# Optimization experiments

Measured on AMD Instinct MI355X. Metric: run time of the kernel, lower is better.

The kernel has to match this reference:

```python
import jax, jax.numpy as jnp
import numpy as np
import math

N, J = 8192, 22  # N = batch*frames (per-frame calls are independent), J = num_joint


def _layernorm(x, g, b, eps=1e-5):
    m = jnp.mean(x, axis=-1, keepdims=True)
    v = jnp.var(x, axis=-1, keepdims=True)
    return (x - m) * jax.lax.rsqrt(v + eps) * g + b


def _attention(x, Wqkv, bqkv, Wo, bo, heads):
    # x: [B, n, d]; matches torch Attention (scale = d**-0.5)
    B, n, d = x.shape
    hd = d // heads
    qkv = (x @ Wqkv + bqkv).reshape(B, n, 3, heads, hd).transpose(2, 0, 3, 1, 4)
    q, k, v = qkv[0], qkv[1], qkv[2]  # [B, h, n, hd]
    dots = jnp.einsum('bhid,bhjd->bhij', q, k) * (d ** -0.5)
    attn = jax.nn.softmax(dots, axis=-1)
    out = jnp.einsum('bhij,bhjd->bhid', attn, v)
    out = out.transpose(0, 2, 1, 3).reshape(B, n, -1)
    return out @ Wo + bo


def _encoder(x, tok_W, tok_b, qkv_W, qkv_b, o_W, o_b, ln_g, ln_b, m1_W, m1_b, m2_W, m2_b, heads):
    tok = x @ tok_W + tok_b                                   # [B, J, 64]
    h = _attention(tok, qkv_W, qkv_b, o_W, o_b, heads)        # [B, J, out_dim]
    hn = _layernorm(h, ln_g, ln_b)
    mlp = jax.nn.relu(hn @ m1_W + m1_b) @ m2_W + m2_b
    return h + mlp                                            # Residual(LN+MLP)


def _sinusoidal_pe(max_len, dim):
    pos = np.arange(max_len)[:, None].astype(np.float32)
    div = np.exp(np.arange(0, dim, 2, dtype=np.float32) * (-math.log(10000.0) / dim))
    pe = np.zeros((max_len, dim), dtype=np.float32)
    pe[:, 0::2] = np.sin(pos * div)
    pe[:, 1::2] = np.cos(pos * div)
    return jnp.asarray(pe)


def setup_inputs() -> dict:
    key = jax.random.key(0)
    ks = iter(jax.random.split(key, 64))
    rn = lambda shape, s=0.1: jax.random.normal(next(ks), shape, dtype=jnp.float32) * s
    inp = {
        'q_t': jax.random.normal(next(ks), (N, J, 4), dtype=jnp.float32),
        'skelA': jax.random.normal(next(ks), (N, J, 3), dtype=jnp.float32),
        'skelB': jax.random.normal(next(ks), (N, J, 3), dtype=jnp.float32),
        'quat_mean': jax.random.normal(next(ks), (J, 4), dtype=jnp.float32) * 0.1,
        'quat_std': jax.random.uniform(next(ks), (J, 4), dtype=jnp.float32, minval=0.5, maxval=1.5),
        # QuatEncoder params
        'qe_tok_W': rn((4, 64)), 'qe_tok_b': jnp.zeros((64,), jnp.float32),
        'qe_qkv_W': rn((64, 192)), 'qe_qkv_b': jnp.zeros((192,), jnp.float32),
        'qe_o_W': rn((64, 256)), 'qe_o_b': jnp.zeros((256,), jnp.float32),
        'qe_ln_g': jnp.ones((256,), jnp.float32), 'qe_ln_b': jnp.zeros((256,), jnp.float32),
        'qe_m1_W': rn((256, 512)), 'qe_m1_b': jnp.zeros((512,), jnp.float32),
        'qe_m2_W': rn((512, 256)), 'qe_m2_b': jnp.zeros((256,), jnp.float32),
        # shared SeklEncoder params
        'se_tok_W': rn((3, 64)), 'se_tok_b': jnp.zeros((64,), jnp.float32),
        'se_qkv_W': rn((64, 192)), 'se_qkv_b': jnp.zeros((192,), jnp.float32),
        'se_o_W': rn((64, 128)), 'se_o_b': jnp.zeros((128,), jnp.float32),
        'se_ln_g': jnp.ones((128,), jnp.float32), 'se_ln_b': jnp.zeros((128,), jnp.float32),
        'se_m1_W': rn((128, 256)), 'se_m1_b': jnp.zeros((256,), jnp.float32),
        'se_m2_W': rn((256, 128)), 'se_m2_b': jnp.zeros((128,), jnp.float32),
        # head
        'emb_W': rn((512, 128)), 'emb_b': jnp.zeros((128,), jnp.float32),
        'del_W': rn((128, 4)), 'del_b': jnp.zeros((4,), jnp.float32),
    }
    return inp


def reference(q_t, skelA, skelB, quat_mean, quat_std,
              qe_tok_W, qe_tok_b, qe_qkv_W, qe_qkv_b, qe_o_W, qe_o_b,
              qe_ln_g, qe_ln_b, qe_m1_W, qe_m1_b, qe_m2_W, qe_m2_b,
              se_tok_W, se_tok_b, se_qkv_W, se_qkv_b, se_o_W, se_o_b,
              se_ln_g, se_ln_b, se_m1_W, se_m1_b, se_m2_W, se_m2_b,
              emb_W, emb_b, del_W, del_b):
    q_embed = _encoder(q_t, qe_tok_W, qe_tok_b, qe_qkv_W, qe_qkv_b, qe_o_W, qe_o_b,
                       qe_ln_g, qe_ln_b, qe_m1_W, qe_m1_b, qe_m2_W, qe_m2_b, heads=4)   # [N,J,256]
    sA = _encoder(skelA, se_tok_W, se_tok_b, se_qkv_W, se_qkv_b, se_o_W, se_o_b,
                  se_ln_g, se_ln_b, se_m1_W, se_m1_b, se_m2_W, se_m2_b, heads=2)        # [N,J,128]
    sB = _encoder(skelB, se_tok_W, se_tok_b, se_qkv_W, se_qkv_b, se_o_W, se_o_b,
                  se_ln_g, se_ln_b, se_m1_W, se_m1_b, se_m2_W, se_m2_b, heads=2)        # [N,J,128]
    cat = jnp.concatenate([q_embed, sA, sB], axis=-1)                                   # [N,J,512]
    dim = cat.shape[-1]
    pe = _sinusoidal_pe(J, dim)
    pos = cat * math.sqrt(dim) + pe[None, :, :]
    embed = jax.nn.relu(pos @ emb_W + emb_b)                                            # [N,J,128]
    delta = embed @ del_W + del_b                                                       # [N,J,4]
    delta = delta * quat_std + quat_mean
    # normalized()
    lengths = jnp.sqrt(jnp.sum(delta * delta, axis=-1, keepdims=True))
    return delta / lengths
```

## Files before the change

kernel.cpp:

```cpp
#include <hip/hip_runtime.h>
#include <hip/hip_bf16.h>
#include <math.h>

#define NJ 22
#define MROWS 44
#define PROWS 48
#define NRT 3

typedef float f4 __attribute__((ext_vector_type(4)));
typedef _Float16 h8 __attribute__((ext_vector_type(8)));

#define WOFF_QE_QKV 0
#define WOFF_QE_O   24576
#define WOFF_QE_M1  57344
#define WOFF_QE_M2  319488
#define WOFF_SE_QKV 581632
#define WOFF_SE_O   606208
#define WOFF_SE_M1  622592
#define WOFF_SE_M2  688128
#define WOFF_EMB    753664

struct Smem {
    _Float16 XH[PROWS * 256];
    __align__(16) char U[PROWS * 128 * 4];
    float LNp[PROWS * 4], LNq[PROWS * 4];
    float LNm[PROWS], LNr[PROWS];
    float Sx[MROWS * 4];
    float Sd[MROWS * 4];
};

struct Args {
    const float *q_t, *skelA, *skelB, *quat_mean, *quat_std;
    const float *qe_tok_W, *qe_tok_b, *qe_qkv_b, *qe_o_b, *qe_ln_g, *qe_ln_b, *qe_m1_b, *qe_m2_b;
    const float *se_tok_W, *se_tok_b, *se_qkv_b, *se_o_b, *se_ln_g, *se_ln_b, *se_m1_b, *se_m2_b;
    const float *del_W, *del_b;
    const float *P;
    const _Float16 *W;
    float *out;
};

__device__ __forceinline__ int swz(int r, int c) {
    return (((c >> 3) ^ (r & 7)) << 3) | (c & 7);
}

template<int NI, int KSTEPS, int LDA>
__device__ __forceinline__ void mfma_gemm(f4 (&acc)[NI][NRT],
        const _Float16 *AH,
        const _Float16 *BH, const _Float16 *BL,
        int wK, int koff, int w, int l) {
    const int m = l & 15, q = l >> 4;
#pragma unroll 1
    for (int s = 0; s < KSTEPS; s++) {
        const int ka = s * 32 + q * 8;
        h8 a[NRT];
#pragma unroll
        for (int rt = 0; rt < NRT; rt++) {
            int r = rt * 16 + m;
            a[rt] = *(const h8 *)(AH + r * LDA + (((ka >> 3) ^ (r & 7)) << 3));
        }
#pragma unroll
        for (int i = 0; i < NI; i++) {
            int n = (w + 4 * i) * 16 + m;
            int boff = n * wK + koff + ka;
            h8 bh = *(const h8 *)(BH + boff);
            h8 bl = *(const h8 *)(BL + boff);
#pragma unroll
            for (int rt = 0; rt < NRT; rt++) {
                acc[i][rt] = __builtin_amdgcn_mfma_f32_16x16x32_f16(a[rt], bh, acc[i][rt], 0, 0, 0);
                acc[i][rt] = __builtin_amdgcn_mfma_f32_16x16x32_f16(a[rt], bl, acc[i][rt], 0, 0, 0);
            }
        }
    }
}

template<int NH, int HD>
__device__ __forceinline__ void attention(Smem &sm, int t) {
    constexpr int SPL = HD / 16;
    if (t < NH * MROWS * SPL) {
        const int half = t & (SPL - 1);
        const int ur = t / SPL;
        const int hh = ur / MROWS;
        const int rr = ur - hh * MROWS;
        const int jb = (rr >= NJ) ? NJ : 0;
        const float *KF = (const float *)sm.U;
        const float *VF = KF + PROWS * 64;
        const int c0 = 64 + hh * HD + half * 16;
        float qv[16];
#pragma unroll
        for (int g = 0; g < 2; g++) {
            h8 qh = *(const h8 *)(sm.XH + rr * 256 + swz(rr, c0 + g * 8));
#pragma unroll
            for (int d = 0; d < 8; d++) qv[g * 8 + d] = (float)qh[d];
        }
        float s[NJ];
        float mx = -1e30f;
#pragma unroll
        for (int j = 0; j < NJ; j++) {
            const float *kp = KF + (jb + j) * 64 + hh * HD + half * 16;
            float acc = 0.f;
#pragma unroll
            for (int d = 0; d < 16; d += 4) {
                float4 v = *(const float4 *)(kp + d);
                acc += qv[d] * v.x + qv[d + 1] * v.y + qv[d + 2] * v.z + qv[d + 3] * v.w;
            }
            if constexpr (SPL == 2) acc += __shfl_xor(acc, 1);
            s[j] = acc * 0.125f;
            mx = fmaxf(mx, s[j]);
        }
        float sum = 0.f;
#pragma unroll
        for (int j = 0; j < NJ; j++) { s[j] = __expf(s[j] - mx); sum += s[j]; }
        float inv = 1.f / sum;
        float o[16];
#pragma unroll
        for (int d = 0; d < 16; d++) o[d] = 0.f;
#pragma unroll
        for (int j = 0; j < NJ; j++) {
            float p = s[j] * inv;
            const float *vp = VF + (jb + j) * 64 + hh * HD + half * 16;
#pragma unroll
            for (int d = 0; d < 16; d += 4) {
                float4 v = *(const float4 *)(vp + d);
                o[d] = fmaf(p, v.x, o[d]);       o[d + 1] = fmaf(p, v.y, o[d + 1]);
                o[d + 2] = fmaf(p, v.z, o[d + 2]); o[d + 3] = fmaf(p, v.w, o[d + 3]);
            }
        }
        const int cw = hh * HD + half * 16;
#pragma unroll
        for (int g = 0; g < 2; g++) {
            h8 oh;
#pragma unroll
            for (int d = 0; d < 8; d++) oh[d] = (_Float16)o[g * 8 + d];
            *(h8 *)(sm.XH + rr * 256 + swz(rr, cw + g * 8)) = oh;
        }
    }
}

template<int D, int NH, int TK>
__device__ __forceinline__ void encode(Smem &sm, const float *__restrict__ xg,
        const float *__restrict__ tokW, const float *__restrict__ tokB,
        const float *__restrict__ qkvB, const float *__restrict__ oB,
        const float *__restrict__ lnG,  const float *__restrict__ lnB,
        const float *__restrict__ m1B,  const float *__restrict__ m2B,
        const _Float16 *__restrict__ Wq,  const _Float16 *__restrict__ Wo,
        const _Float16 *__restrict__ Wm1, const _Float16 *__restrict__ Wm2,
        const _Float16 *__restrict__ Wemb, int embKoff,
        f4 (&emb)[2][NRT], int t, int w, int l) {
    constexpr int NI = D / 64;
    constexpr int HID = 2 * D;
    const int m = l & 15, q = l >> 4;

    if (t < MROWS * TK) sm.Sx[t] = xg[t];
    __syncthreads();
    {
        float b = tokB[l];
#pragma unroll
        for (int i = 0; i < 11; i++) {
            int r = w + 4 * i;
            float acc = b;
#pragma unroll
            for (int k = 0; k < TK; k++)
                acc = fmaf(sm.Sx[r * TK + k], tokW[k * 64 + l], acc);
            sm.XH[r * 256 + swz(r, l)] = (_Float16)acc;
        }
    }
    __syncthreads();
    {
        f4 acc[3][NRT];
#pragma unroll
        for (int i = 0; i < 3; i++)
#pragma unroll
            for (int rt = 0; rt < NRT; rt++) acc[i][rt] = (f4){0.f, 0.f, 0.f, 0.f};
        mfma_gemm<3, 2, 256>(acc, sm.XH, Wq, Wq + 192 * 64, 64, 0, w, l);
        float *KV = (float *)sm.U;
#pragma unroll
        for (int i = 0; i < 3; i++) {
            int c = (w + 4 * i) * 16 + m;
            float b = qkvB[c];
#pragma unroll
            for (int rt = 0; rt < NRT; rt++)
#pragma unroll
                for (int e = 0; e < 4; e++) {
                    int r = rt * 16 + q * 4 + e;
                    float v = acc[i][rt][e] + b;
                    sm.XH[r * 256 + swz(r, 64 + c)] = (_Float16)v;
                    if (c >= 128)      KV[PROWS * 64 + r * 64 + (c - 128)] = v;
                    else if (c >= 64)  KV[r * 64 + (c - 64)] = v;
                }
        }
    }
    __syncthreads();
    attention<NH, 64 / NH>(sm, t);
    __syncthreads();
    f4 res[NI][NRT];
#pragma unroll
    for (int i = 0; i < NI; i++)
#pragma unroll
        for (int rt = 0; rt < NRT; rt++) res[i][rt] = (f4){0.f, 0.f, 0.f, 0.f};
    mfma_gemm<NI, 2, 256>(res, sm.XH, Wo, Wo + D * 64, 64, 0, w, l);
#pragma unroll
    for (int i = 0; i < NI; i++) {
        float b = oB[(w + 4 * i) * 16 + m];
#pragma unroll
        for (int rt = 0; rt < NRT; rt++)
#pragma unroll
            for (int e = 0; e < 4; e++) res[i][rt][e] += b;
    }
#pragma unroll
    for (int rt = 0; rt < NRT; rt++)
#pragma unroll
        for (int e = 0; e < 4; e++) {
            int r = rt * 16 + q * 4 + e;
            float s1 = 0.f, s2 = 0.f;
#pragma unroll
            for (int i = 0; i < NI; i++) {
                float v = res[i][rt][e];
                s1 += v; s2 = fmaf(v, v, s2);
            }
#pragma unroll
            for (int off = 8; off > 0; off >>= 1) {
                s1 += __shfl_xor(s1, off);
                s2 += __shfl_xor(s2, off);
            }
            if (m == 0) { sm.LNp[r * 4 + w] = s1; sm.LNq[r * 4 + w] = s2; }
        }
    __syncthreads();
    if (t < PROWS) {
        float s1 = sm.LNp[t * 4] + sm.LNp[t * 4 + 1] + sm.LNp[t * 4 + 2] + sm.LNp[t * 4 + 3];
        float s2 = sm.LNq[t * 4] + sm.LNq[t * 4 + 1] + sm.LNq[t * 4 + 2] + sm.LNq[t * 4 + 3];
        float mean = s1 * (1.f / D);
        float var = s2 * (1.f / D) - mean * mean;
        sm.LNm[t] = mean;
        sm.LNr[t] = rsqrtf(fmaxf(var, 0.f) + 1e-5f);
    }
    __syncthreads();
#pragma unroll
    for (int i = 0; i < NI; i++) {
        int c = (w + 4 * i) * 16 + m;
        float g = lnG[c], bb = lnB[c];
#pragma unroll
        for (int rt = 0; rt < NRT; rt++)
#pragma unroll
            for (int e = 0; e < 4; e++) {
                int r = rt * 16 + q * 4 + e;
                float v = (res[i][rt][e] - sm.LNm[r]) * sm.LNr[r] * g + bb;
                sm.XH[r * 256 + swz(r, c)] = (_Float16)v;
            }
    }
    __syncthreads();
    _Float16 *HH = (_Float16 *)sm.U;
#pragma unroll 1
    for (int cb = 0; cb < HID / 128; cb++) {
        f4 h1[2][NRT];
#pragma unroll
        for (int i = 0; i < 2; i++)
#pragma unroll
            for (int rt = 0; rt < NRT; rt++) h1[i][rt] = (f4){0.f, 0.f, 0.f, 0.f};
        mfma_gemm<2, D / 32, 256>(h1, sm.XH,
                                  Wm1 + cb * 128 * D, Wm1 + HID * D + cb * 128 * D, D, 0, w, l);
        __syncthreads();
#pragma unroll
        for (int i = 0; i < 2; i++) {
            int c = (w + 4 * i) * 16 + m;
            float b = m1B[cb * 128 + c];
#pragma unroll
            for (int rt = 0; rt < NRT; rt++)
#pragma unroll
                for (int e = 0; e < 4; e++) {
                    int r = rt * 16 + q * 4 + e;
                    HH[r * 128 + swz(r, c)] = (_Float16)fmaxf(h1[i][rt][e] + b, 0.f);
                }
        }
        __syncthreads();
        mfma_gemm<NI, 4, 128>(res, HH, Wm2, Wm2 + D * HID, HID, cb * 128, w, l);
    }
    __syncthreads();
#pragma unroll
    for (int i = 0; i < NI; i++) {
        int c = (w + 4 * i) * 16 + m;
        float b = m2B[c];
#pragma unroll
        for (int rt = 0; rt < NRT; rt++)
#pragma unroll
            for (int e = 0; e < 4; e++) {
                int r = rt * 16 + q * 4 + e;
                sm.XH[r * 256 + swz(r, c)] = (_Float16)(res[i][rt][e] + b);
            }
    }
    __syncthreads();
    mfma_gemm<2, D / 32, 256>(emb, sm.XH, Wemb, Wemb + 128 * 512, 512, embKoff, w, l);
}

__global__ __launch_bounds__(256, 2) void fused_kernel(Args A) {
    __shared__ __align__(16) Smem sm;
    const int t = threadIdx.x, w = t >> 6, l = t & 63;
    const int m = l & 15, q = l >> 4;
    const int blk = blockIdx.x;

    for (int i = t; i < 4 * 256; i += 256) {
        int r = MROWS + (i >> 8), c = i & 255;
        sm.XH[r * 256 + c] = (_Float16)0.f;
    }

    f4 emb[2][NRT];
#pragma unroll
    for (int i = 0; i < 2; i++)
#pragma unroll
        for (int rt = 0; rt < NRT; rt++) emb[i][rt] = (f4){0.f, 0.f, 0.f, 0.f};

    const _Float16 *W = A.W;
    const _Float16 *Wemb = W + WOFF_EMB;

    encode<256, 4, 4>(sm, A.q_t + blk * MROWS * 4,
                      A.qe_tok_W, A.qe_tok_b, A.qe_qkv_b, A.qe_o_b,
                      A.qe_ln_g, A.qe_ln_b, A.qe_m1_b, A.qe_m2_b,
                      W + WOFF_QE_QKV, W + WOFF_QE_O, W + WOFF_QE_M1, W + WOFF_QE_M2,
                      Wemb, 0, emb, t, w, l);
    encode<128, 2, 3>(sm, A.skelA + blk * MROWS * 3,
                      A.se_tok_W, A.se_tok_b, A.se_qkv_b, A.se_o_b,
                      A.se_ln_g, A.se_ln_b, A.se_m1_b, A.se_m2_b,
                      W + WOFF_SE_QKV, W + WOFF_SE_O, W + WOFF_SE_M1, W + WOFF_SE_M2,
                      Wemb, 256, emb, t, w, l);
    encode<128, 2, 3>(sm, A.skelB + blk * MROWS * 3,
                      A.se_tok_W, A.se_tok_b, A.se_qkv_b, A.se_o_b,
                      A.se_ln_g, A.se_ln_b, A.se_m1_b, A.se_m2_b,
                      W + WOFF_SE_QKV, W + WOFF_SE_O, W + WOFF_SE_M1, W + WOFF_SE_M2,
                      Wemb, 384, emb, t, w, l);

    __syncthreads();
    float *E = (float *)sm.U;
#pragma unroll
    for (int i = 0; i < 2; i++) {
        int c = (w + 4 * i) * 16 + m;
#pragma unroll
        for (int rt = 0; rt < NRT; rt++)
#pragma unroll
            for (int e = 0; e < 4; e++) {
                int r = rt * 16 + q * 4 + e;
                int j = (r >= NJ) ? r - NJ : r;
                j = (j >= NJ) ? 0 : j;
                float v = fmaf(22.627416997969522f, emb[i][rt][e], A.P[j * 128 + c]);
                E[r * 128 + c] = fmaxf(v, 0.f);
            }
    }
    __syncthreads();
    if (t < MROWS * 4) {
        int r = t >> 2, d = t & 3;
        float acc = A.del_b[d];
        for (int c = 0; c < 128; c++)
            acc = fmaf(E[r * 128 + c], A.del_W[c * 4 + d], acc);
        int j = (r >= NJ) ? r - NJ : r;
        acc = fmaf(acc, A.quat_std[j * 4 + d], A.quat_mean[j * 4 + d]);
        sm.Sd[t] = acc;
    }
    __syncthreads();
    if (t < MROWS * 4) {
        int r = t >> 2;
        float x0 = sm.Sd[r * 4], x1 = sm.Sd[r * 4 + 1];
        float x2 = sm.Sd[r * 4 + 2], x3 = sm.Sd[r * 4 + 3];
        float inv = 1.f / sqrtf(x0 * x0 + x1 * x1 + x2 * x2 + x3 * x3);
        A.out[blk * MROWS * 4 + t] = sm.Sd[t] * inv;
    }
}

struct WDesc { const float *W; int K; int N; int off; };
struct SplitArgs { WDesc d[9]; _Float16 *out; };

__global__ void split_kernel(SplitArgs a) {
    WDesc d = a.d[blockIdx.y];
    int e = blockIdx.x * 256 + threadIdx.x;
    int tot = d.K * d.N;
    if (e < tot) {
        int n = e / d.K, k = e - n * d.K;
        float v = d.W[k * d.N + n];
        _Float16 h = (_Float16)v;
        a.out[d.off + e] = h;
        a.out[d.off + tot + e] = (_Float16)(v - (float)h);
    }
}

__global__ void pe_emb_kernel(const float *__restrict__ emb_W,
                              const float *__restrict__ emb_b, float *P) {
    int r = blockIdx.x;
    int c = threadIdx.x;
    float acc = emb_b[c];
    const float k = -2.f * logf(10000.f) / 512.f;
    for (int i = 0; i < 256; i++) {
        float ang = (float)r * expf((float)i * k);
        acc = fmaf(sinf(ang), emb_W[(2 * i) * 128 + c], acc);
        acc = fmaf(cosf(ang), emb_W[(2 * i + 1) * 128 + c], acc);
    }
    P[r * 128 + c] = acc;
}

extern "C" void kernel_launch(void *const *d_in, const int *in_sizes, int n_in,
                              void *d_out, int out_size, void *d_ws, size_t ws_size,
                              hipStream_t stream) {
    const float **in = (const float **)d_in;
    float *P = (float *)d_ws;
    _Float16 *W = (_Float16 *)((float *)d_ws + 22 * 128);

    Args A;
    A.q_t = in[0]; A.skelA = in[1]; A.skelB = in[2]; A.quat_mean = in[3]; A.quat_std = in[4];
    A.qe_tok_W = in[5]; A.qe_tok_b = in[6]; A.qe_qkv_b = in[8]; A.qe_o_b = in[10];
    A.qe_ln_g = in[11]; A.qe_ln_b = in[12]; A.qe_m1_b = in[14]; A.qe_m2_b = in[16];
    A.se_tok_W = in[17]; A.se_tok_b = in[18]; A.se_qkv_b = in[20]; A.se_o_b = in[22];
    A.se_ln_g = in[23]; A.se_ln_b = in[24]; A.se_m1_b = in[26]; A.se_m2_b = in[28];
    A.del_W = in[31]; A.del_b = in[32];
    A.P = P; A.W = W; A.out = (float *)d_out;

    SplitArgs sa;
    sa.d[0] = { in[7],  64, 192, WOFF_QE_QKV };
    sa.d[1] = { in[9],  64, 256, WOFF_QE_O };
    sa.d[2] = { in[13], 256, 512, WOFF_QE_M1 };
    sa.d[3] = { in[15], 512, 256, WOFF_QE_M2 };
    sa.d[4] = { in[19], 64, 192, WOFF_SE_QKV };
    sa.d[5] = { in[21], 64, 128, WOFF_SE_O };
    sa.d[6] = { in[25], 128, 256, WOFF_SE_M1 };
    sa.d[7] = { in[27], 256, 128, WOFF_SE_M2 };
    sa.d[8] = { in[29], 512, 128, WOFF_EMB };
    sa.out = W;

    int n_items = in_sizes[0] / (NJ * 4);
    int blocks = n_items / 2;

    split_kernel<<<dim3(512, 9), 256, 0, stream>>>(sa);
    pe_emb_kernel<<<NJ, 128, 0, stream>>>(in[29], in[30], P);
    fused_kernel<<<blocks, 256, 0, stream>>>(A);
}
```

Measured before the change: 1.376 ms.

## Split embedding head into separate kernel via fp16 concat buffer in global memory

The fused encoder kernel now writes each encoder's output as fp16 into a global concat buffer instead of accumulating the 512→128 embedding GEMM in registers. A new head_kernel processes 64-row tiles with MFMA, reading A rows directly from global memory, then applies PE bias, ReLU, the delta projection and normalization. The aim is to cut register pressure and barriers in the main kernel and to run the head GEMM at fuller 64-row tiles instead of 44 padded rows. The cost is a global round-trip of about 8192×22×512 fp16 values plus an extra launch.

```diff
diff --git a/kernel.cpp b/kernel.cpp
--- a/kernel.cpp
+++ b/kernel.cpp
@@ -19,6 +19,7 @@
 #define WOFF_SE_M1  622592
 #define WOFF_SE_M2  688128
 #define WOFF_EMB    753664
+#define W_TOTAL     884736
 
 struct Smem {
     _Float16 XH[PROWS * 256];
@@ -26,7 +27,6 @@
     float LNp[PROWS * 4], LNq[PROWS * 4];
     float LNm[PROWS], LNr[PROWS];
     float Sx[MROWS * 4];
-    float Sd[MROWS * 4];
 };
 
 struct Args {
@@ -36,6 +36,7 @@
     const float *del_W, *del_b;
     const float *P;
     const _Float16 *W;
+    _Float16 *cat;
     float *out;
 };
 
@@ -144,8 +145,7 @@
         const float *__restrict__ m1B,  const float *__restrict__ m2B,
         const _Float16 *__restrict__ Wq,  const _Float16 *__restrict__ Wo,
         const _Float16 *__restrict__ Wm1, const _Float16 *__restrict__ Wm2,
-        const _Float16 *__restrict__ Wemb, int embKoff,
-        f4 (&emb)[2][NRT], int t, int w, int l) {
+        _Float16 *__restrict__ catb, int catoff, int t, int w, int l) {
     constexpr int NI = D / 64;
     constexpr int HID = 2 * D;
     const int m = l & 15, q = l >> 4;
@@ -274,7 +274,6 @@
         __syncthreads();
         mfma_gemm<NI, 4, 128>(res, HH, Wm2, Wm2 + D * HID, HID, cb * 128, w, l);
     }
-    __syncthreads();
 #pragma unroll
     for (int i = 0; i < NI; i++) {
         int c = (w + 4 * i) * 16 + m;
@@ -284,17 +283,15 @@
 #pragma unroll
             for (int e = 0; e < 4; e++) {
                 int r = rt * 16 + q * 4 + e;
-                sm.XH[r * 256 + swz(r, c)] = (_Float16)(res[i][rt][e] + b);
-            }
-    }
-    __syncthreads();
-    mfma_gemm<2, D / 32, 256>(emb, sm.XH, Wemb, Wemb + 128 * 512, 512, embKoff, w, l);
+                if (r < MROWS)
+                    catb[r * 512 + catoff + c] = (_Float16)(res[i][rt][e] + b);
+            }
+    }
 }
 
 __global__ __launch_bounds__(256, 2) void fused_kernel(Args A) {
     __shared__ __align__(16) Smem sm;
     const int t = threadIdx.x, w = t >> 6, l = t & 63;
-    const int m = l & 15, q = l >> 4;
     const int blk = blockIdx.x;
 
     for (int i = t; i < 4 * 256; i += 256) {
@@ -302,64 +299,113 @@
         sm.XH[r * 256 + c] = (_Float16)0.f;
     }
 
-    f4 emb[2][NRT];
-#pragma unroll
-    for (int i = 0; i < 2; i++)
-#pragma unroll
-        for (int rt = 0; rt < NRT; rt++) emb[i][rt] = (f4){0.f, 0.f, 0.f, 0.f};
-
     const _Float16 *W = A.W;
-    const _Float16 *Wemb = W + WOFF_EMB;
+    _Float16 *catb = A.cat + (size_t)blk * MROWS * 512;
 
     encode<256, 4, 4>(sm, A.q_t + blk * MROWS * 4,
                       A.qe_tok_W, A.qe_tok_b, A.qe_qkv_b, A.qe_o_b,
                       A.qe_ln_g, A.qe_ln_b, A.qe_m1_b, A.qe_m2_b,
                       W + WOFF_QE_QKV, W + WOFF_QE_O, W + WOFF_QE_M1, W + WOFF_QE_M2,
-                      Wemb, 0, emb, t, w, l);
+                      catb, 0, t, w, l);
     encode<128, 2, 3>(sm, A.skelA + blk * MROWS * 3,
                       A.se_tok_W, A.se_tok_b, A.se_qkv_b, A.se_o_b,
                       A.se_ln_g, A.se_ln_b, A.se_m1_b, A.se_m2_b,
                       W + WOFF_SE_QKV, W + WOFF_SE_O, W + WOFF_SE_M1, W + WOFF_SE_M2,
-                      Wemb, 256, emb, t, w, l);
+                      catb, 256, t, w, l);
     encode<128, 2, 3>(sm, A.skelB + blk * MROWS * 3,
                       A.se_tok_W, A.se_tok_b, A.se_qkv_b, A.se_o_b,
                       A.se_ln_g, A.se_ln_b, A.se_m1_b, A.se_m2_b,
                       W + WOFF_SE_QKV, W + WOFF_SE_O, W + WOFF_SE_M1, W + WOFF_SE_M2,
-                      Wemb, 384, emb, t, w, l);
-
-    __syncthreads();
-    float *E = (float *)sm.U;
+                      catb, 384, t, w, l);
+}
+
+struct HeadArgs {
+    const _Float16 *cat;
+    const _Float16 *W;
+    const float *P;
+    const float *del_W, *del_b, *quat_mean, *quat_std;
+    float *out;
+    int R;
+};
+
+#define ELD 132
+
+__global__ __launch_bounds__(256, 4) void head_kernel(HeadArgs A) {
+    __shared__ float E[64 * ELD];
+    __shared__ float Sd[64 * 4];
+    const int t = threadIdx.x, w = t >> 6, l = t & 63;
+    const int m = l & 15, q = l >> 4;
+    const int rowbase = blockIdx.x * 64;
+    const _Float16 *BH = A.W + WOFF_EMB;
+    const _Float16 *BL = BH + 128 * 512;
+
+    f4 acc[2][4];
+#pragma unroll
+    for (int i = 0; i < 2; i++)
+#pragma unroll
+        for (int rt = 0; rt < 4; rt++) acc[i][rt] = (f4){0.f, 0.f, 0.f, 0.f};
+
+#pragma unroll 1
+    for (int s = 0; s < 16; s++) {
+        const int ka = s * 32 + q * 8;
+        h8 a[4];
+#pragma unroll
+        for (int rt = 0; rt < 4; rt++) {
+            int rg = rowbase + rt * 16 + m;
+            rg = rg < A.R ? rg : A.R - 1;
+            a[rt] = *(const h8 *)(A.cat + (size_t)rg * 512 + ka);
+        }
+#pragma unroll
+        for (int i = 0; i < 2; i++) {
+            int n = (w + 4 * i) * 16 + m;
+            h8 bh = *(const h8 *)(BH + n * 512 + ka);
+            h8 bl = *(const h8 *)(BL + n * 512 + ka);
+#pragma unroll
+            for (int rt = 0; rt < 4; rt++) {
+                acc[i][rt] = __builtin_amdgcn_mfma_f32_16x16x32_f16(a[rt], bh, acc[i][rt], 0, 0, 0);
+                acc[i][rt] = __builtin_amdgcn_mfma_f32_16x16x32_f16(a[rt], bl, acc[i][rt], 0, 0, 0);
+            }
+        }
+    }
 #pragma unroll
     for (int i = 0; i < 2; i++) {
         int c = (w + 4 * i) * 16 + m;
 #pragma unroll
-        for (int rt = 0; rt < NRT; rt++)
+        for (int rt = 0; rt < 4; rt++)
 #pragma unroll
             for (int e = 0; e < 4; e++) {
                 int r = rt * 16 + q * 4 + e;
-                int j = (r >= NJ) ? r - NJ : r;
-                j = (j >= NJ) ? 0 : j;
-                float v = fmaf(22.627416997969522f, emb[i][rt][e], A.P[j * 128 + c]);
-                E[r * 128 + c] = fmaxf(v, 0.f);
-            }
-    }
-    __syncthreads();
-    if (t < MROWS * 4) {
+                int j = (rowbase + r) % NJ;
+                float v = fmaf(22.627416997969522f, acc[i][rt][e], A.P[j * 128 + c]);
+                E[r * ELD + c] = fmaxf(v, 0.f);
+            }
+    }
+    __syncthreads();
+    {
         int r = t >> 2, d = t & 3;
-        float acc = A.del_b[d];
-        for (int c = 0; c < 128; c++)
-            acc = fmaf(E[r * 128 + c], A.del_W[c * 4 + d], acc);
-        int j = (r >= NJ) ? r - NJ : r;
-        acc = fmaf(acc, A.quat_std[j * 4 + d], A.quat_mean[j * 4 + d]);
-        sm.Sd[t] = acc;
-    }
-    __syncthreads();
-    if (t < MROWS * 4) {
+        float a2 = A.del_b[d];
+        const float *Er = E + r * ELD;
+#pragma unroll 4
+        for (int c4 = 0; c4 < 32; c4++) {
+            float4 ev = *(const float4 *)(Er + c4 * 4);
+            a2 = fmaf(ev.x, A.del_W[(c4 * 4 + 0) * 4 + d], a2);
+            a2 = fmaf(ev.y, A.del_W[(c4 * 4 + 1) * 4 + d], a2);
+            a2 = fmaf(ev.z, A.del_W[(c4 * 4 + 2) * 4 + d], a2);
+            a2 = fmaf(ev.w, A.del_W[(c4 * 4 + 3) * 4 + d], a2);
+        }
+        int j = (rowbase + r) % NJ;
+        Sd[t] = fmaf(a2, A.quat_std[j * 4 + d], A.quat_mean[j * 4 + d]);
+    }
+    __syncthreads();
+    {
         int r = t >> 2;
-        float x0 = sm.Sd[r * 4], x1 = sm.Sd[r * 4 + 1];
-        float x2 = sm.Sd[r * 4 + 2], x3 = sm.Sd[r * 4 + 3];
-        float inv = 1.f / sqrtf(x0 * x0 + x1 * x1 + x2 * x2 + x3 * x3);
-        A.out[blk * MROWS * 4 + t] = sm.Sd[t] * inv;
+        int rg = rowbase + r;
+        if (rg < A.R) {
+            float x0 = Sd[r * 4], x1 = Sd[r * 4 + 1];
+            float x2 = Sd[r * 4 + 2], x3 = Sd[r * 4 + 3];
+            float inv = 1.f / sqrtf(x0 * x0 + x1 * x1 + x2 * x2 + x3 * x3);
+            A.out[(size_t)rg * 4 + (t & 3)] = Sd[t] * inv;
+        }
     }
 }
 
@@ -399,6 +445,7 @@
     const float **in = (const float **)d_in;
     float *P = (float *)d_ws;
     _Float16 *W = (_Float16 *)((float *)d_ws + 22 * 128);
+    _Float16 *cat = W + W_TOTAL;
 
     Args A;
     A.q_t = in[0]; A.skelA = in[1]; A.skelB = in[2]; A.quat_mean = in[3]; A.quat_std = in[4];
@@ -407,7 +454,7 @@
     A.se_tok_W = in[17]; A.se_tok_b = in[18]; A.se_qkv_b = in[20]; A.se_o_b = in[22];
     A.se_ln_g = in[23]; A.se_ln_b = in[24]; A.se_m1_b = in[26]; A.se_m2_b = in[28];
     A.del_W = in[31]; A.del_b = in[32];
-    A.P = P; A.W = W; A.out = (float *)d_out;
+    A.P = P; A.W = W; A.cat = cat; A.out = (float *)d_out;
 
     SplitArgs sa;
     sa.d[0] = { in[7],  64, 192, WOFF_QE_QKV };
@@ -423,8 +470,15 @@
 
     int n_items = in_sizes[0] / (NJ * 4);
     int blocks = n_items / 2;
+    int R = n_items * NJ;
+
+    HeadArgs H;
+    H.cat = cat; H.W = W; H.P = P;
+    H.del_W = in[31]; H.del_b = in[32]; H.quat_mean = in[3]; H.quat_std = in[4];
+    H.out = (float *)d_out; H.R = R;
 
     split_kernel<<<dim3(512, 9), 256, 0, stream>>>(sa);
     pe_emb_kernel<<<NJ, 128, 0, stream>>>(in[29], in[30], P);
     fused_kernel<<<blocks, 256, 0, stream>>>(A);
-}
+    head_kernel<<<(R + 63) / 64, 256, 0, stream>>>(H);
+}
```

Result: no change. 1.383 ms (+0.5%).
